# Kernel optimization log

Measured on AMD Instinct MI355X. Metric: run time of the kernel, lower is better.

## Reference

```python
import jax, jax.numpy as jnp
import numpy as np

N_BLOCKS = 8
HIDDEN = 256
BATCH = 4096
IN_DIM = 3 * N_BLOCKS


def setup_inputs() -> dict:
    key = jax.random.key(0)
    ks = jax.random.split(key, 32)
    s = 0.05
    d = {}
    d['x'] = jax.random.normal(ks[0], (BATCH, IN_DIM), dtype=jnp.float32)
    # per-block object encoders (stacked): in -> H, relu, H -> H, relu, H -> H
    d['o_W0'] = jax.random.normal(ks[1], (N_BLOCKS, IN_DIM, HIDDEN), dtype=jnp.float32) * s
    d['o_b0'] = jnp.zeros((N_BLOCKS, HIDDEN), jnp.float32)
    d['o_W1'] = jax.random.normal(ks[2], (N_BLOCKS, HIDDEN, HIDDEN), dtype=jnp.float32) * s
    d['o_b1'] = jnp.zeros((N_BLOCKS, HIDDEN), jnp.float32)
    d['o_W2'] = jax.random.normal(ks[3], (N_BLOCKS, HIDDEN, HIDDEN), dtype=jnp.float32) * s
    d['o_b2'] = jnp.zeros((N_BLOCKS, HIDDEN), jnp.float32)
    # clear predicate encoder: H -> H, relu, H -> H, relu, H -> 1, sigmoid
    d['c_W0'] = jax.random.normal(ks[4], (HIDDEN, HIDDEN), dtype=jnp.float32) * s
    d['c_b0'] = jnp.zeros((HIDDEN,), jnp.float32)
    d['c_W1'] = jax.random.normal(ks[5], (HIDDEN, HIDDEN), dtype=jnp.float32) * s
    d['c_b1'] = jnp.zeros((HIDDEN,), jnp.float32)
    d['c_W2'] = jax.random.normal(ks[6], (HIDDEN, 1), dtype=jnp.float32) * s
    d['c_b2'] = jnp.zeros((1,), jnp.float32)
    # ontable predicate encoder
    d['t_W0'] = jax.random.normal(ks[7], (HIDDEN, HIDDEN), dtype=jnp.float32) * s
    d['t_b0'] = jnp.zeros((HIDDEN,), jnp.float32)
    d['t_W1'] = jax.random.normal(ks[8], (HIDDEN, HIDDEN), dtype=jnp.float32) * s
    d['t_b1'] = jnp.zeros((HIDDEN,), jnp.float32)
    d['t_W2'] = jax.random.normal(ks[9], (HIDDEN, 1), dtype=jnp.float32) * s
    d['t_b2'] = jnp.zeros((1,), jnp.float32)
    # AonB predicate encoder: 2H -> H, relu, H -> H, relu, H -> 1, sigmoid
    d['a_W0'] = jax.random.normal(ks[10], (2 * HIDDEN, HIDDEN), dtype=jnp.float32) * s
    d['a_b0'] = jnp.zeros((HIDDEN,), jnp.float32)
    d['a_W1'] = jax.random.normal(ks[11], (HIDDEN, HIDDEN), dtype=jnp.float32) * s
    d['a_b1'] = jnp.zeros((HIDDEN,), jnp.float32)
    d['a_W2'] = jax.random.normal(ks[12], (HIDDEN, 1), dtype=jnp.float32) * s
    d['a_b2'] = jnp.zeros((1,), jnp.float32)
    return d


def _pred_mlp(h, W0, b0, W1, b1, W2, b2):
    h = jax.nn.relu(h @ W0 + b0)
    h = jax.nn.relu(h @ W1 + b1)
    return jax.nn.sigmoid(h @ W2 + b2)


def reference(x, o_W0, o_b0, o_W1, o_b1, o_W2, o_b2,
              c_W0, c_b0, c_W1, c_b1, c_W2, c_b2,
              t_W0, t_b0, t_W1, t_b1, t_W2, t_b2,
              a_W0, a_b0, a_W1, a_b1, a_W2, a_b2):
    B = x.shape[0]
    H = o_W0.shape[-1]
    # object encodings: (N, B, H), all N encoders batched via einsum
    h = jax.nn.relu(jnp.einsum('bd,ndh->nbh', x, o_W0) + o_b0[:, None, :])
    h = jax.nn.relu(jnp.einsum('nbh,nhk->nbk', h, o_W1) + o_b1[:, None, :])
    enc = jnp.einsum('nbh,nhk->nbk', h, o_W2) + o_b2[:, None, :]
    # clear/ontable predicates: (N, B, 1) -> (B, N)
    clear = _pred_mlp(enc, c_W0, c_b0, c_W1, c_b1, c_W2, c_b2)[..., 0].T
    table = _pred_mlp(enc, t_W0, t_b0, t_W1, t_b1, t_W2, t_b2)[..., 0].T
    # AonB over all pairs; split first layer to avoid materializing (N,N,B,2H)
    a_l = jnp.einsum('nbh,hk->nbk', enc, a_W0[:H])
    a_r = jnp.einsum('nbh,hk->nbk', enc, a_W0[H:])
    ph = jax.nn.relu(a_l[:, None] + a_r[None, :] + a_b0)  # (N, N, B, H), axis0=i(left), axis1=j(right)
    ph = jax.nn.relu(ph @ a_W1 + a_b1)
    aonb = jax.nn.sigmoid(ph @ a_W2 + a_b2)[..., 0]  # (N, N, B)
    aonb_b = jnp.transpose(aonb, (2, 0, 1))  # (B, N, N)
    # per block i: [AonB(i,0..N-1), clear(i), ontable(i)] concatenated over i
    out = jnp.concatenate([aonb_b, clear[..., None], table[..., None]], axis=2)
    return out.reshape(B, -1)
```

## Files before the change

### kernel.cpp

```cpp
#include <hip/hip_runtime.h>
#include <hip/hip_bf16.h>

#define OFF_O0   0u
#define OFF_O1   65536u
#define OFF_O2   589824u
#define OFF_C0   1114112u
#define OFF_C1   1179648u
#define OFF_T0   1245184u
#define OFF_T1   1310720u
#define OFF_AL   1376256u
#define OFF_AR   1441792u
#define OFF_A1   1507328u
#define OFF_ENC  1572864u
#define OFF_ALQ  9961472u
#define OFF_ARQ  18350080u

typedef short s8v __attribute__((ext_vector_type(8)));
typedef float f4v __attribute__((ext_vector_type(4)));

__device__ __forceinline__ unsigned short f2bf(float f) {
  unsigned u = __float_as_uint(f);
  unsigned r = (u + 0x7FFFu + ((u >> 16) & 1u)) >> 16;
  return (unsigned short)r;
}
__device__ __forceinline__ float bf2f(unsigned short h) {
  return __uint_as_float(((unsigned)h) << 16);
}

__device__ __forceinline__ void gemm_epilogue(
    f4v acc[4][4], const float* bias, int act,
    unsigned short* outb, unsigned short* gout)
{
  int lane = threadIdx.x & 63;
  int w    = threadIdx.x >> 6;
  int lr = lane & 15, kh = lane >> 4;
  if (outb) __syncthreads();
  #pragma unroll
  for (int nt = 0; nt < 4; nt++) {
    int col = w*64 + nt*16 + lr;
    float bv = bias ? bias[col] : 0.0f;
    #pragma unroll
    for (int mt = 0; mt < 4; mt++) {
      #pragma unroll
      for (int i = 0; i < 4; i++) {
        int row = mt*16 + kh*4 + i;
        float v = acc[mt][nt][i] + bv;
        if (act) v = fmaxf(v, 0.0f);
        unsigned short hh = f2bf(v);
        if (outb) {
          int bofs = (2*col) ^ ((row & 7) << 4);
          *(unsigned short*)((char*)outb + row*512 + bofs) = hh;
        }
        if (gout) gout[row*256 + col] = hh;
      }
    }
  }
  if (outb) __syncthreads();
}

__device__ __forceinline__ void gemm_core(
    const unsigned short* inb, const unsigned short* __restrict__ wt,
    f4v acc[4][4])
{
  int lane = threadIdx.x & 63;
  int w    = threadIdx.x >> 6;
  int lr = lane & 15, kh = lane >> 4;
  #pragma unroll
  for (int a = 0; a < 4; a++)
    #pragma unroll
    for (int b = 0; b < 4; b++) acc[a][b] = (f4v){0.f,0.f,0.f,0.f};
  #pragma unroll
  for (int k0 = 0; k0 < 256; k0 += 32) {
    s8v bfrag[4];
    #pragma unroll
    for (int nt = 0; nt < 4; nt++)
      bfrag[nt] = *(const s8v*)(wt + (w*64 + nt*16 + lr)*256 + k0 + kh*8);
    #pragma unroll
    for (int mt = 0; mt < 4; mt++) {
      int row = mt*16 + lr;
      int bofs = (2*k0 + kh*16) ^ ((row & 7) << 4);
      s8v afrag = *(const s8v*)((const char*)inb + row*512 + bofs);
      #pragma unroll
      for (int nt = 0; nt < 4; nt++)
        acc[mt][nt] = __builtin_amdgcn_mfma_f32_16x16x32_bf16(afrag, bfrag[nt], acc[mt][nt], 0, 0, 0);
    }
  }
}

__device__ __forceinline__ void gemm64(
    const unsigned short* inb, const unsigned short* __restrict__ wt,
    const float* bias, int act, unsigned short* outb, unsigned short* gout)
{
  f4v acc[4][4];
  gemm_core(inb, wt, acc);
  gemm_epilogue(acc, bias, act, outb, gout);
}

__device__ __forceinline__ void dot_tail(
    f4v acc[4][4], const float* __restrict__ bias,
    const float* __restrict__ w2, float b2,
    float* __restrict__ out, int m0, int offs, float* red)
{
  int lane = threadIdx.x & 63;
  int w    = threadIdx.x >> 6;
  int lr = lane & 15, kh = lane >> 4;
  float w2v[4], bv[4];
  #pragma unroll
  for (int nt = 0; nt < 4; nt++) {
    int col = w*64 + nt*16 + lr;
    w2v[nt] = w2[col];
    bv[nt]  = bias[col];
  }
  #pragma unroll
  for (int mt = 0; mt < 4; mt++) {
    #pragma unroll
    for (int i = 0; i < 4; i++) {
      float s = 0.0f;
      #pragma unroll
      for (int nt = 0; nt < 4; nt++)
        s += fmaxf(acc[mt][nt][i] + bv[nt], 0.0f) * w2v[nt];
      s += __shfl_xor(s, 1);
      s += __shfl_xor(s, 2);
      s += __shfl_xor(s, 4);
      s += __shfl_xor(s, 8);
      if (lr == 0) red[(mt*16 + kh*4 + i)*4 + w] = s;
    }
  }
  __syncthreads();
  if (threadIdx.x < 64) {
    int row = threadIdx.x;
    float s = red[row*4] + red[row*4+1] + red[row*4+2] + red[row*4+3];
    out[(m0 + row)*80 + offs] = 1.0f / (1.0f + __expf(-s - b2));
  }
}

__device__ __forceinline__ void gemm_x(
    const unsigned short* xb, const unsigned short* __restrict__ wt,
    const float* bias, unsigned short* outb)
{
  int lane = threadIdx.x & 63;
  int w    = threadIdx.x >> 6;
  int lr = lane & 15, kh = lane >> 4;
  f4v acc[4][4];
  #pragma unroll
  for (int a = 0; a < 4; a++)
    #pragma unroll
    for (int b = 0; b < 4; b++) acc[a][b] = (f4v){0.f,0.f,0.f,0.f};

  s8v bfrag[4];
  #pragma unroll
  for (int nt = 0; nt < 4; nt++)
    bfrag[nt] = *(const s8v*)(wt + (w*64 + nt*16 + lr)*32 + kh*8);
  #pragma unroll
  for (int mt = 0; mt < 4; mt++) {
    s8v afrag = *(const s8v*)(xb + (mt*16 + lr)*32 + kh*8);
    #pragma unroll
    for (int nt = 0; nt < 4; nt++)
      acc[mt][nt] = __builtin_amdgcn_mfma_f32_16x16x32_bf16(afrag, bfrag[nt], acc[mt][nt], 0, 0, 0);
  }
  gemm_epilogue(acc, bias, 1, outb, nullptr);
}

__global__ __launch_bounds__(256) void prep_kernel(
    const float* __restrict__ oW0, const float* __restrict__ oW1,
    const float* __restrict__ oW2, const float* __restrict__ cW0,
    const float* __restrict__ cW1, const float* __restrict__ tW0,
    const float* __restrict__ tW1, const float* __restrict__ aW0,
    const float* __restrict__ aW1, unsigned short* __restrict__ ws)
{
  __shared__ float t[32][33];
  int b = blockIdx.x;
  if (b < 1472) {
    int m = b >> 6, tile = b & 63;
    const float* src; unsigned short* dst;
    if      (m < 8)  { src = oW1 + m*65536;       dst = ws + OFF_O1 + m*65536; }
    else if (m < 16) { src = oW2 + (m-8)*65536;   dst = ws + OFF_O2 + (m-8)*65536; }
    else if (m == 16){ src = cW0;                 dst = ws + OFF_C0; }
    else if (m == 17){ src = cW1;                 dst = ws + OFF_C1; }
    else if (m == 18){ src = tW0;                 dst = ws + OFF_T0; }
    else if (m == 19){ src = tW1;                 dst = ws + OFF_T1; }
    else if (m == 20){ src = aW1;                 dst = ws + OFF_A1; }
    else if (m == 21){ src = aW0;                 dst = ws + OFF_AL; }
    else             { src = aW0 + 65536;         dst = ws + OFF_AR; }
    int kt = tile & 7, nt = tile >> 3;
    int tx = threadIdx.x & 31, ty = threadIdx.x >> 5;
    #pragma unroll
    for (int r = 0; r < 4; r++) {
      int ky = ty*4 + r;
      t[ky][tx] = src[(kt*32 + ky)*256 + nt*32 + tx];
    }
    __syncthreads();
    #pragma unroll
    for (int r = 0; r < 4; r++) {
      int ny = ty*4 + r;
      dst[(nt*32 + ny)*256 + kt*32 + tx] = f2bf(t[tx][ny]);
    }
  } else {
    int idx = (b - 1472)*256 + threadIdx.x;
    int k = idx & 31, n2 = (idx >> 5) & 255, nb = idx >> 13;
    float v = (k < 24) ? oW0[(nb*24 + k)*256 + n2] : 0.0f;
    ws[OFF_O0 + idx] = f2bf(v);
  }
}

__global__ __launch_bounds__(256) void encoder_kernel(
    const float* __restrict__ x,
    const float* __restrict__ ob0, const float* __restrict__ ob1,
    const float* __restrict__ ob2, const float* __restrict__ ab0,
    unsigned short* __restrict__ ws)
{
  __shared__ unsigned short buf[64*256];
  __shared__ unsigned short xb[64*32];
  int n  = blockIdx.x >> 6;
  int m0 = (blockIdx.x & 63) * 64;

  for (int t = threadIdx.x; t < 64*32; t += 256) {
    int row = t >> 5, c = t & 31;
    xb[t] = f2bf(c < 24 ? x[(m0 + row)*24 + c] : 0.0f);
  }
  __syncthreads();
  gemm_x (xb,  ws + OFF_O0 + n*8192,  ob0 + n*256, buf);
  gemm64 (buf, ws + OFF_O1 + n*65536, ob1 + n*256, 1, buf, nullptr);
  gemm64 (buf, ws + OFF_O2 + n*65536, ob2 + n*256, 0, buf,
          ws + OFF_ENC + (unsigned)(n*4096 + m0)*256);
  gemm64 (buf, ws + OFF_AL, nullptr, 0, nullptr,
          ws + OFF_ALQ + (unsigned)(n*4096 + m0)*256);
  gemm64 (buf, ws + OFF_AR, ab0, 0, nullptr,
          ws + OFF_ARQ + (unsigned)(n*4096 + m0)*256);
}

__global__ __launch_bounds__(256) void pair_kernel(
    const unsigned short* __restrict__ ws,
    const float* __restrict__ ab1, const float* __restrict__ aW2,
    const float* __restrict__ ab2, float* __restrict__ out)
{
  __shared__ unsigned short wlds[256*256];
  __shared__ unsigned short ph[2][32*256];
  int b    = blockIdx.x;
  int i    = b >> 5;
  int cset = b & 31;
  int tid  = threadIdx.x;
  int lane = tid & 63, w = tid >> 6;
  int lr = lane & 15, kh = lane >> 4;

  {
    const unsigned short* wt = ws + OFF_A1;
    #pragma unroll
    for (int it = 0; it < 32; it++) {
      int idx = it*256 + tid;
      int row = idx >> 5, c8 = idx & 31;
      s8v v = *(const s8v*)(wt + row*256 + c8*8);
      *(s8v*)((char*)wlds + row*512 + ((c8*16) ^ ((row & 7) << 4))) = v;
    }
  }
  float w2v[4], bv[4];
  #pragma unroll
  for (int nt = 0; nt < 4; nt++) {
    int col = w*64 + nt*16 + lr;
    w2v[nt] = aW2[col];
    bv[nt]  = ab1[col];
  }
  float b2 = ab2[0];

  const unsigned short* Lbase = ws + OFF_ALQ + (unsigned)i*4096u*256u;
  const unsigned short* Rbase = ws + OFF_ARQ;

  int srow[4], sc8[4];
  #pragma unroll
  for (int q = 0; q < 4; q++) {
    int idx = q*256 + tid;
    srow[q] = idx >> 5; sc8[q] = idx & 31;
  }

  {
    const unsigned short* Lp = Lbase + (unsigned)(cset*4 + 0)*32u*256u;
    const unsigned short* Rp = Rbase + (unsigned)(cset*4 + 0)*32u*256u;
    #pragma unroll
    for (int q = 0; q < 4; q++) {
      s8v l8 = *(const s8v*)(Lp + srow[q]*256 + sc8[q]*8);
      s8v r8 = *(const s8v*)(Rp + srow[q]*256 + sc8[q]*8);
      s8v o8;
      #pragma unroll
      for (int e = 0; e < 8; e++) {
        float v = bf2f((unsigned short)l8[e]) + bf2f((unsigned short)r8[e]);
        o8[e] = (short)f2bf(fmaxf(v, 0.0f));
      }
      *(s8v*)((char*)ph[0] + srow[q]*512 + ((sc8[q]*16) ^ ((srow[q] & 7) << 4))) = o8;
    }
  }
  __syncthreads();

  int cur = 0;
  for (int t = 0; t < 32; t++) {
    int c = t >> 3, j = t & 7;
    s8v Lr[4], Rr[4];
    if (t < 31) {
      int t1 = t + 1;
      int c1 = t1 >> 3, j1 = t1 & 7;
      const unsigned short* Lp = Lbase + (unsigned)(cset*4 + c1)*32u*256u;
      const unsigned short* Rp = Rbase + ((unsigned)j1*4096u + (cset*4 + c1)*32u)*256u;
      #pragma unroll
      for (int q = 0; q < 4; q++) {
        Lr[q] = *(const s8v*)(Lp + srow[q]*256 + sc8[q]*8);
        Rr[q] = *(const s8v*)(Rp + srow[q]*256 + sc8[q]*8);
      }
    }
    f4v acc[2][4];
    #pragma unroll
    for (int a = 0; a < 2; a++)
      #pragma unroll
      for (int cc = 0; cc < 4; cc++) acc[a][cc] = (f4v){0.f,0.f,0.f,0.f};
    const unsigned short* inb = ph[cur];
    #pragma unroll
    for (int k0 = 0; k0 < 256; k0 += 32) {
      s8v bfrag[4];
      #pragma unroll
      for (int nt = 0; nt < 4; nt++) {
        int row = w*64 + nt*16 + lr;
        int bofs = (2*k0 + kh*16) ^ ((row & 7) << 4);
        bfrag[nt] = *(const s8v*)((const char*)wlds + row*512 + bofs);
      }
      #pragma unroll
      for (int mt = 0; mt < 2; mt++) {
        int row = mt*16 + lr;
        int bofs = (2*k0 + kh*16) ^ ((row & 7) << 4);
        s8v afrag = *(const s8v*)((const char*)inb + row*512 + bofs);
        #pragma unroll
        for (int nt = 0; nt < 4; nt++)
          acc[mt][nt] = __builtin_amdgcn_mfma_f32_16x16x32_bf16(afrag, bfrag[nt], acc[mt][nt], 0, 0, 0);
      }
    }
    if (t < 31) {
      #pragma unroll
      for (int q = 0; q < 4; q++) {
        s8v o8;
        #pragma unroll
        for (int e = 0; e < 8; e++) {
          float v = bf2f((unsigned short)Lr[q][e]) + bf2f((unsigned short)Rr[q][e]);
          o8[e] = (short)f2bf(fmaxf(v, 0.0f));
        }
        *(s8v*)((char*)ph[cur ^ 1] + srow[q]*512 + ((sc8[q]*16) ^ ((srow[q] & 7) << 4))) = o8;
      }
    }
    __syncthreads();
    float* red = (float*)ph[cur];
    #pragma unroll
    for (int mt = 0; mt < 2; mt++) {
      #pragma unroll
      for (int ii = 0; ii < 4; ii++) {
        float s = 0.0f;
        #pragma unroll
        for (int nt = 0; nt < 4; nt++)
          s += fmaxf(acc[mt][nt][ii] + bv[nt], 0.0f) * w2v[nt];
        s += __shfl_xor(s, 1);
        s += __shfl_xor(s, 2);
        s += __shfl_xor(s, 4);
        s += __shfl_xor(s, 8);
        if (lr == 0) red[(mt*16 + kh*4 + ii)*4 + w] = s;
      }
    }
    __syncthreads();
    if (tid < 32) {
      float s = red[tid*4] + red[tid*4+1] + red[tid*4+2] + red[tid*4+3];
      out[((cset*4 + c)*32 + tid)*80 + i*10 + j] = 1.0f / (1.0f + __expf(-s - b2));
    }
    __syncthreads();
    cur ^= 1;
  }
}

__global__ __launch_bounds__(256) void pred_kernel(
    const unsigned short* __restrict__ ws,
    const float* __restrict__ cb0, const float* __restrict__ cb1,
    const float* __restrict__ cW2, const float* __restrict__ cb2,
    const float* __restrict__ tb0, const float* __restrict__ tb1,
    const float* __restrict__ tW2, const float* __restrict__ tb2,
    float* __restrict__ out)
{
  __shared__ unsigned short bufA[64*256];
  __shared__ float red[256];
  int b  = blockIdx.x;
  int p  = b >> 9;
  int n  = (b >> 6) & 7;
  int m0 = (b & 63) * 64;
  const unsigned short* encp = ws + OFF_ENC + (unsigned)(n*4096 + m0)*256;
  for (int t = threadIdx.x; t < 64*32; t += 256) {
    int row = t >> 5, chunk = t & 31;
    s8v v = *(const s8v*)(encp + row*256 + chunk*8);
    int bofs = (chunk*16) ^ ((row & 7) << 4);
    *(s8v*)((char*)bufA + row*512 + bofs) = v;
  }
  __syncthreads();
  const unsigned short* W0 = ws + (p ? OFF_T0 : OFF_C0);
  const unsigned short* W1 = ws + (p ? OFF_T1 : OFF_C1);
  gemm64(bufA, W0, p ? tb0 : cb0, 1, bufA, nullptr);
  f4v acc[4][4];
  gemm_core(bufA, W1, acc);
  dot_tail(acc, p ? tb1 : cb1, p ? tW2 : cW2,
           p ? tb2[0] : cb2[0], out, m0, n*10 + 8 + p, red);
}

extern "C" void kernel_launch(void* const* d_in, const int* in_sizes, int n_in,
                              void* d_out, int out_size, void* d_ws, size_t ws_size,
                              hipStream_t stream) {
  (void)in_sizes; (void)n_in; (void)out_size; (void)ws_size;
  const float* x   = (const float*)d_in[0];
  const float* oW0 = (const float*)d_in[1];
  const float* ob0 = (const float*)d_in[2];
  const float* oW1 = (const float*)d_in[3];
  const float* ob1 = (const float*)d_in[4];
  const float* oW2 = (const float*)d_in[5];
  const float* ob2 = (const float*)d_in[6];
  const float* cW0 = (const float*)d_in[7];
  const float* cb0 = (const float*)d_in[8];
  const float* cW1 = (const float*)d_in[9];
  const float* cb1 = (const float*)d_in[10];
  const float* cW2 = (const float*)d_in[11];
  const float* cb2 = (const float*)d_in[12];
  const float* tW0 = (const float*)d_in[13];
  const float* tb0 = (const float*)d_in[14];
  const float* tW1 = (const float*)d_in[15];
  const float* tb1 = (const float*)d_in[16];
  const float* tW2 = (const float*)d_in[17];
  const float* tb2 = (const float*)d_in[18];
  const float* aW0 = (const float*)d_in[19];
  const float* ab0 = (const float*)d_in[20];
  const float* aW1 = (const float*)d_in[21];
  const float* ab1 = (const float*)d_in[22];
  const float* aW2 = (const float*)d_in[23];
  const float* ab2 = (const float*)d_in[24];
  unsigned short* ws = (unsigned short*)d_ws;
  float* out = (float*)d_out;

  hipLaunchKernelGGL(prep_kernel, dim3(1728), dim3(256), 0, stream,
                     oW0, oW1, oW2, cW0, cW1, tW0, tW1, aW0, aW1, ws);
  hipLaunchKernelGGL(encoder_kernel, dim3(512), dim3(256), 0, stream,
                     x, ob0, ob1, ob2, ab0, ws);
  hipLaunchKernelGGL(pair_kernel, dim3(256), dim3(256), 0, stream,
                     ws, ab1, aW2, ab2, out);
  hipLaunchKernelGGL(pred_kernel, dim3(1024), dim3(256), 0, stream,
                     ws, cb0, cb1, cW2, cb2, tb0, tb1, tW2, tb2, out);
}
```

Baseline: 207.0 us.

## Restructure pair kernel: 64-row tiles, 512 threads, weights read from global

```diff
diff --git a/kernel.cpp b/kernel.cpp
--- a/kernel.cpp
+++ b/kernel.cpp
@@ -229,121 +229,99 @@
           ws + OFF_ARQ + (unsigned)(n*4096 + m0)*256);
 }
 
-__global__ __launch_bounds__(256) void pair_kernel(
+__global__ __launch_bounds__(512) void pair_kernel(
     const unsigned short* __restrict__ ws,
     const float* __restrict__ ab1, const float* __restrict__ aW2,
     const float* __restrict__ ab2, float* __restrict__ out)
 {
-  __shared__ unsigned short wlds[256*256];
-  __shared__ unsigned short ph[2][32*256];
-  int b    = blockIdx.x;
-  int i    = b >> 5;
-  int cset = b & 31;
+  __shared__ unsigned short ph[2][64*256];
+  __shared__ float red[2][256];
+  int b = blockIdx.x;
+  int i = b >> 6, chunk = b & 63;
+  int m0 = chunk * 64;
+  const unsigned short* Lp    = ws + OFF_ALQ + ((unsigned)i*4096u + m0)*256u;
+  const unsigned short* Rbase = ws + OFF_ARQ + (unsigned)m0*256u;
+  const unsigned short* wt    = ws + OFF_A1;
+
   int tid  = threadIdx.x;
   int lane = tid & 63, w = tid >> 6;
+  int wm = w >> 2, wn = w & 3;
   int lr = lane & 15, kh = lane >> 4;
 
-  {
-    const unsigned short* wt = ws + OFF_A1;
-    #pragma unroll
-    for (int it = 0; it < 32; it++) {
-      int idx = it*256 + tid;
-      int row = idx >> 5, c8 = idx & 31;
-      s8v v = *(const s8v*)(wt + row*256 + c8*8);
-      *(s8v*)((char*)wlds + row*512 + ((c8*16) ^ ((row & 7) << 4))) = v;
-    }
-  }
+  int srow[4], sc8[4];
+  #pragma unroll
+  for (int q = 0; q < 4; q++) {
+    int idx = q*512 + tid;
+    srow[q] = idx >> 5; sc8[q] = idx & 31;
+  }
+
   float w2v[4], bv[4];
   #pragma unroll
   for (int nt = 0; nt < 4; nt++) {
-    int col = w*64 + nt*16 + lr;
+    int col = wn*64 + nt*16 + lr;
     w2v[nt] = aW2[col];
     bv[nt]  = ab1[col];
   }
   float b2 = ab2[0];
 
-  const unsigned short* Lbase = ws + OFF_ALQ + (unsigned)i*4096u*256u;
-  const unsigned short* Rbase = ws + OFF_ARQ;
-
-  int srow[4], sc8[4];
   #pragma unroll
   for (int q = 0; q < 4; q++) {
-    int idx = q*256 + tid;
-    srow[q] = idx >> 5; sc8[q] = idx & 31;
-  }
-
-  {
-    const unsigned short* Lp = Lbase + (unsigned)(cset*4 + 0)*32u*256u;
-    const unsigned short* Rp = Rbase + (unsigned)(cset*4 + 0)*32u*256u;
-    #pragma unroll
-    for (int q = 0; q < 4; q++) {
-      s8v l8 = *(const s8v*)(Lp + srow[q]*256 + sc8[q]*8);
-      s8v r8 = *(const s8v*)(Rp + srow[q]*256 + sc8[q]*8);
-      s8v o8;
-      #pragma unroll
-      for (int e = 0; e < 8; e++) {
-        float v = bf2f((unsigned short)l8[e]) + bf2f((unsigned short)r8[e]);
-        o8[e] = (short)f2bf(fmaxf(v, 0.0f));
-      }
-      *(s8v*)((char*)ph[0] + srow[q]*512 + ((sc8[q]*16) ^ ((srow[q] & 7) << 4))) = o8;
-    }
+    unsigned off = (unsigned)srow[q]*256u + sc8[q]*8;
+    s8v l8 = *(const s8v*)(Lp + off);
+    s8v r8 = *(const s8v*)(Rbase + off);
+    s8v o8;
+    #pragma unroll
+    for (int e = 0; e < 8; e++) {
+      float v = bf2f((unsigned short)l8[e]) + bf2f((unsigned short)r8[e]);
+      o8[e] = (short)f2bf(fmaxf(v, 0.0f));
+    }
+    *(s8v*)((char*)ph[0] + srow[q]*512 + ((sc8[q]*16) ^ ((srow[q] & 7) << 4))) = o8;
   }
   __syncthreads();
 
-  int cur = 0;
-  for (int t = 0; t < 32; t++) {
-    int c = t >> 3, j = t & 7;
-    s8v Lr[4], Rr[4];
-    if (t < 31) {
-      int t1 = t + 1;
-      int c1 = t1 >> 3, j1 = t1 & 7;
-      const unsigned short* Lp = Lbase + (unsigned)(cset*4 + c1)*32u*256u;
-      const unsigned short* Rp = Rbase + ((unsigned)j1*4096u + (cset*4 + c1)*32u)*256u;
-      #pragma unroll
-      for (int q = 0; q < 4; q++) {
-        Lr[q] = *(const s8v*)(Lp + srow[q]*256 + sc8[q]*8);
-        Rr[q] = *(const s8v*)(Rp + srow[q]*256 + sc8[q]*8);
-      }
+  int c = 0;
+  for (int j = 0; j < 8; j++) {
+    s8v Rr[4];
+    if (j < 7) {
+      const unsigned short* Rp = Rbase + (unsigned)(j+1)*(4096u*256u);
+      #pragma unroll
+      for (int q = 0; q < 4; q++)
+        Rr[q] = *(const s8v*)(Rp + (unsigned)srow[q]*256u + sc8[q]*8);
     }
     f4v acc[2][4];
     #pragma unroll
     for (int a = 0; a < 2; a++)
       #pragma unroll
       for (int cc = 0; cc < 4; cc++) acc[a][cc] = (f4v){0.f,0.f,0.f,0.f};
-    const unsigned short* inb = ph[cur];
     #pragma unroll
     for (int k0 = 0; k0 < 256; k0 += 32) {
       s8v bfrag[4];
       #pragma unroll
-      for (int nt = 0; nt < 4; nt++) {
-        int row = w*64 + nt*16 + lr;
+      for (int nt = 0; nt < 4; nt++)
+        bfrag[nt] = *(const s8v*)(wt + (wn*64 + nt*16 + lr)*256 + k0 + kh*8);
+      #pragma unroll
+      for (int mt = 0; mt < 2; mt++) {
+        int row = wm*32 + mt*16 + lr;
         int bofs = (2*k0 + kh*16) ^ ((row & 7) << 4);
-        bfrag[nt] = *(const s8v*)((const char*)wlds + row*512 + bofs);
-      }
-      #pragma unroll
-      for (int mt = 0; mt < 2; mt++) {
-        int row = mt*16 + lr;
-        int bofs = (2*k0 + kh*16) ^ ((row & 7) << 4);
-        s8v afrag = *(const s8v*)((const char*)inb + row*512 + bofs);
+        s8v afrag = *(const s8v*)((const char*)ph[c] + row*512 + bofs);
         #pragma unroll
         for (int nt = 0; nt < 4; nt++)
           acc[mt][nt] = __builtin_amdgcn_mfma_f32_16x16x32_bf16(afrag, bfrag[nt], acc[mt][nt], 0, 0, 0);
       }
     }
-    if (t < 31) {
+    if (j < 7) {
       #pragma unroll
       for (int q = 0; q < 4; q++) {
+        s8v l8 = *(const s8v*)(Lp + (unsigned)srow[q]*256u + sc8[q]*8);
         s8v o8;
         #pragma unroll
         for (int e = 0; e < 8; e++) {
-          float v = bf2f((unsigned short)Lr[q][e]) + bf2f((unsigned short)Rr[q][e]);
+          float v = bf2f((unsigned short)l8[e]) + bf2f((unsigned short)Rr[q][e]);
           o8[e] = (short)f2bf(fmaxf(v, 0.0f));
         }
-        *(s8v*)((char*)ph[cur ^ 1] + srow[q]*512 + ((sc8[q]*16) ^ ((srow[q] & 7) << 4))) = o8;
+        *(s8v*)((char*)ph[c ^ 1] + srow[q]*512 + ((sc8[q]*16) ^ ((srow[q] & 7) << 4))) = o8;
       }
     }
-    __syncthreads();
-    float* red = (float*)ph[cur];
     #pragma unroll
     for (int mt = 0; mt < 2; mt++) {
       #pragma unroll
@@ -356,16 +334,15 @@
         s += __shfl_xor(s, 2);
         s += __shfl_xor(s, 4);
         s += __shfl_xor(s, 8);
-        if (lr == 0) red[(mt*16 + kh*4 + ii)*4 + w] = s;
+        if (lr == 0) red[c][(wm*32 + mt*16 + kh*4 + ii)*4 + wn] = s;
       }
     }
     __syncthreads();
-    if (tid < 32) {
-      float s = red[tid*4] + red[tid*4+1] + red[tid*4+2] + red[tid*4+3];
-      out[((cset*4 + c)*32 + tid)*80 + i*10 + j] = 1.0f / (1.0f + __expf(-s - b2));
-    }
-    __syncthreads();
-    cur ^= 1;
+    if (tid < 64) {
+      float s = red[c][tid*4] + red[c][tid*4+1] + red[c][tid*4+2] + red[c][tid*4+3];
+      out[(m0 + tid)*80 + i*10 + j] = 1.0f / (1.0f + __expf(-s - b2));
+    }
+    c ^= 1;
   }
 }
 
@@ -436,7 +413,7 @@
                      oW0, oW1, oW2, cW0, cW1, tW0, tW1, aW0, aW1, ws);
   hipLaunchKernelGGL(encoder_kernel, dim3(512), dim3(256), 0, stream,
                      x, ob0, ob1, ob2, ab0, ws);
-  hipLaunchKernelGGL(pair_kernel, dim3(256), dim3(256), 0, stream,
+  hipLaunchKernelGGL(pair_kernel, dim3(512), dim3(512), 0, stream,
                      ws, ab1, aW2, ab2, out);
   hipLaunchKernelGGL(pred_kernel, dim3(1024), dim3(256), 0, stream,
                      ws, cb0, cb1, cW2, cb2, tb0, tb1, tW2, tb2, out);
```

After: 181.8 us (median of 2 runs). 1.14x faster.
